# Kernel optimization log

Hardware: AMD Instinct MI355X
Metric: run time of the kernel (lower is better)

Reference implementation:

```python
import jax, jax.numpy as jnp
import numpy as np

B, N_PER, DEG, F_IN, F_HID = 64, 1024, 16, 128, 128
E = B * N_PER * DEG  # 1,048,576 edges, grouped per graph


def setup_inputs() -> dict:
    key = jax.random.key(0)
    ks = jax.random.split(key, 16)
    n_total = B * N_PER
    x = jax.random.normal(ks[0], (n_total, F_IN), dtype=jnp.float32)
    # edges are random within each graph block
    local = jax.random.randint(ks[1], (2, E), 0, N_PER)
    offs = (jnp.arange(E, dtype=jnp.int64) // (N_PER * DEG)) * N_PER
    edge_index = (local.astype(jnp.int64) + offs[None, :])
    edge_weight = jax.random.uniform(ks[2], (E,), dtype=jnp.float32)
    batch_index = jnp.repeat(jnp.arange(B, dtype=jnp.int64), N_PER)
    s = 1.0 / np.sqrt(F_HID)
    params = {
        'W1': jax.random.normal(ks[3], (F_IN, F_HID)) * s,
        'b1': jnp.zeros((F_HID,), jnp.float32),
        'p1': jax.random.normal(ks[4], (F_HID,)) * s,
        'W2': jax.random.normal(ks[5], (F_HID, F_HID)) * s,
        'b2': jnp.zeros((F_HID,), jnp.float32),
        'p2': jax.random.normal(ks[6], (F_HID,)) * s,
        'W3': jax.random.normal(ks[7], (F_HID, F_HID)) * s,
        'b3': jnp.zeros((F_HID,), jnp.float32),
        'p3': jax.random.normal(ks[8], (F_HID,)) * s,
        'Wo': jax.random.normal(ks[9], (2 * F_HID, 1)) * s,
        'bo': jnp.zeros((1,), jnp.float32),
    }
    return {'x': x, 'edge_index': edge_index, 'edge_weight': edge_weight,
            'batch_index': batch_index, **params}


def _gcn_conv(x, src, dst, w, W, b):
    # GCNConv with add_self_loops=True, symmetric normalization, edge_weight.
    n = x.shape[0]
    xW = x @ W
    deg = jnp.zeros((n,), x.dtype).at[dst].add(w) + 1.0  # +1 from self-loop fill
    dinv = jax.lax.rsqrt(deg)
    norm = dinv[src] * w * dinv[dst]
    agg = jnp.zeros_like(xW).at[dst].add(norm[:, None] * xW[src])
    return agg + (dinv * dinv)[:, None] * xW + b  # self-loop term + bias


def _topk_pool(x, src, dst, w, p, n, k):
    # TopKPooling with nonlinearity=sigmoid, equal-size graphs (n -> k nodes).
    f = x.shape[1]
    xr = x.reshape(B, n, f)
    score = jax.nn.sigmoid((xr @ p) / jnp.linalg.norm(p))  # [B, n]
    vals, perm = jax.lax.top_k(score, k)                    # per-graph top-k
    xn = jnp.take_along_axis(xr, perm[:, :, None], axis=1) * vals[:, :, None]
    # inverse map old local idx -> new local idx (-1 if dropped)
    inv = jnp.full((B, n), -1, dtype=jnp.int32)
    inv = inv.at[jnp.arange(B)[:, None], perm].set(jnp.arange(k, dtype=jnp.int32)[None, :])
    g = src // n
    sl = inv[g, src % n]
    dl = inv[dst // n, dst % n]
    keep = (sl >= 0) & (dl >= 0)
    # dropped edges are masked to node 0 with weight 0 (contribute nothing)
    src2 = jnp.where(keep, g * k + sl, 0)
    dst2 = jnp.where(keep, (dst // n) * k + dl, 0)
    w2 = jnp.where(keep, w, jnp.zeros((), w.dtype))
    return xn.reshape(B * k, f), src2, dst2, w2


def reference(x, edge_index, edge_weight, batch_index,
              W1, b1, p1, W2, b2, p2, W3, b3, p3, Wo, bo):
    src, dst = edge_index[0], edge_index[1]
    w = edge_weight
    n = N_PER
    h = _gcn_conv(x, src, dst, w, W1, b1)
    h, src, dst, w = _topk_pool(h, src, dst, w, p1, n, n // 2); n //= 2
    h = jax.nn.relu(h)
    h = _gcn_conv(h, src, dst, w, W2, b2)
    h, src, dst, w = _topk_pool(h, src, dst, w, p2, n, n // 2); n //= 2
    h = jax.nn.relu(h)
    h = _gcn_conv(h, src, dst, w, W3, b3)
    h, src, dst, w = _topk_pool(h, src, dst, w, p3, n, n // 2); n //= 2
    h = jax.nn.relu(h)
    hr = h.reshape(B, n, -1)
    cat = jnp.concatenate([hr.max(axis=1), hr.mean(axis=1)], axis=1)  # gmp || gap
    out = jax.nn.sigmoid(cat @ Wo + bo)
    return out, cat
```

## Files before the change

### kernel.cpp

```cpp
#include <hip/hip_runtime.h>

#define NB 64
#define EDGES 1048576
#define NTOT  65536

struct __align__(8) CsrE { int s; float w; };

using bf16x8 = __attribute__((ext_vector_type(8))) short;
using f32x4  = __attribute__((ext_vector_type(4))) float;

__global__ void k_zerof(float* __restrict__ p, int n){
  int i=blockIdx.x*256+threadIdx.x; if(i<n) p[i]=0.f;
}

__device__ inline void split1(float x, unsigned &hi16, unsigned &lo16){
  unsigned b=__float_as_uint(x);
  unsigned h=(b+0x7FFFu+((b>>16)&1u))&0xFFFF0000u;
  float lf=x-__uint_as_float(h);
  unsigned lb=__float_as_uint(lf);
  hi16=h>>16;
  lo16=(lb+0x7FFFu+((lb>>16)&1u))>>16;
}

__device__ inline void split8(const float4&u, const float4&v, bf16x8&hi, bf16x8&lo){
  float e[8]={u.x,u.y,u.z,u.w,v.x,v.y,v.z,v.w};
  #pragma unroll
  for(int j=0;j<8;++j){
    unsigned h16,l16; split1(e[j],h16,l16);
    hi[j]=(short)h16; lo[j]=(short)l16;
  }
}

__global__ __launch_bounds__(256) void k_cntpack(const int* __restrict__ edst,
        const float* __restrict__ ew, int* __restrict__ chunkcnt, float* __restrict__ chunkw,
        const float* __restrict__ W1, const float* __restrict__ W2,
        const float* __restrict__ W3, unsigned* __restrict__ outp){
  __shared__ int lc[1024];
  __shared__ float lw[1024];
  int b=blockIdx.x, tid=threadIdx.x;
  if(b<512){
    int xcd=b&7, slot=b>>3;
    int graph=xcd*8+(slot&7), chunk=slot>>3;
    int e0=graph*16384+chunk*2048;
    for(int t=tid;t<1024;t+=256){ lc[t]=0; lw[t]=0.f; }
    __syncthreads();
    for(int e=e0+tid; e<e0+2048; e+=256){
      int dl=edst[e]&1023;
      atomicAdd(&lc[dl],1);
      atomicAdd(&lw[dl],ew[e]);
    }
    __syncthreads();
    for(int t=tid;t<1024;t+=256){
      chunkcnt[chunk*65536+graph*1024+t]=lc[t];
      chunkw  [chunk*65536+graph*1024+t]=lw[t];
    }
  } else {
    int wb=b-512, m=wb>>3;
    const float* W = (m==0)?W1:((m==1)?W2:W3);
    unsigned* o = outp + m*16384;
    for(int t=(wb&7)*256+tid; t<8192; t+=2048){
      int i=t&3, l=(t>>2)&63, c=(t>>8)&7, q=(t>>11)&3;
      int col=c*16+(l&15);
      int k0=q*32+((l>>4)<<3)+i*2;
      float x0=W[k0*128+col], x1=W[(k0+1)*128+col];
      unsigned h0,l0,h1,l1;
      split1(x0,h0,l0); split1(x1,h1,l1);
      int base=((q*8+c)*2)*256;
      o[base + l*4 + i]       = (h1<<16)|h0;
      o[base + 256 + l*4 + i] = (l1<<16)|l0;
    }
  }
}

__global__ __launch_bounds__(256) void k_mm1scat(const float* __restrict__ X,
        const unsigned* __restrict__ Wpk,
        const int* __restrict__ esrc, const int* __restrict__ edst,
        const float* __restrict__ ew, const int* __restrict__ chunkcnt,
        const float* __restrict__ chunkw, int* __restrict__ rowptr,
        float* __restrict__ dinv1, CsrE* __restrict__ csr,
        float* __restrict__ Y){
  __shared__ __align__(16) unsigned Wl[4096];
  int b=blockIdx.x;
  if(b<512){
    const int RPB=128;
    int row0b=b*RPB;
    const int wave=threadIdx.x>>6, lane=threadIdx.x&63;
    const int row0=row0b+wave*32;
    const int lrow=lane&15, lko=(lane>>4)<<3;
    int orow[2];
    #pragma unroll
    for(int s=0;s<2;++s) orow[s]=row0+s*16+lrow;
    const f32x4 vzero={0.f,0.f,0.f,0.f};
    f32x4 acc[2][8];
    #pragma unroll
    for(int s=0;s<2;++s){
      #pragma unroll
      for(int c=0;c<8;++c) acc[s][c]=vzero;
    }
    const char* wb=(const char*)Wl + lane*16;
    float4 u[2],v[2];
    #pragma unroll
    for(int s=0;s<2;++s){
      const float* xp=X+(size_t)orow[s]*128+lko;
      u[s]=*(const float4*)xp; v[s]=*(const float4*)(xp+4);
    }
    #pragma unroll
    for(int q=0;q<4;++q){
      if(q) __syncthreads();
      for(int t=threadIdx.x;t<1024;t+=256)
        ((uint4*)Wl)[t]=((const uint4*)Wpk)[q*1024+t];
      __syncthreads();
      float4 un[2],vn[2];
      if(q<3){
        #pragma unroll
        for(int s=0;s<2;++s){
          const float* xp=X+(size_t)orow[s]*128+(q+1)*32+lko;
          un[s]=*(const float4*)xp; vn[s]=*(const float4*)(xp+4);
        }
      }
      bf16x8 Ah[2],Al[2];
      #pragma unroll
      for(int s=0;s<2;++s) split8(u[s],v[s],Ah[s],Al[s]);
      #pragma unroll
      for(int c=0;c<8;++c){
        const bf16x8 bh=*(const bf16x8*)(wb + c*2048);
        const bf16x8 bl=*(const bf16x8*)(wb + c*2048 + 1024);
        #pragma unroll
        for(int s=0;s<2;++s){
          acc[s][c]=__builtin_amdgcn_mfma_f32_16x16x32_bf16(Ah[s],bh,acc[s][c],0,0,0);
          acc[s][c]=__builtin_amdgcn_mfma_f32_16x16x32_bf16(Al[s],bh,acc[s][c],0,0,0);
          acc[s][c]=__builtin_amdgcn_mfma_f32_16x16x32_bf16(Ah[s],bl,acc[s][c],0,0,0);
        }
      }
      if(q<3){
        #pragma unroll
        for(int s=0;s<2;++s){ u[s]=un[s]; v[s]=vn[s]; }
      }
    }
    const int dcol=lane&15, dr0=(lane>>4)<<2;
    #pragma unroll
    for(int s=0;s<2;++s){
      #pragma unroll
      for(int c=0;c<8;++c){
        #pragma unroll
        for(int r=0;r<4;++r){
          Y[(size_t)(row0+s*16+dr0+r)*128 + c*16 + dcol]=acc[s][c][r];
        }
      }
    }
  } else {
    int* lc=(int*)Wl;
    int* wsum=(int*)Wl+1024;
    int sb=b-512, i=threadIdx.x;
    int lane=i&63, w=i>>6;
    int xcd=sb&7, slot=sb>>3;
    int graph=xcd*8+(slot&7), chunk=slot>>3;
    int n0=4*i, o0=graph*1024+n0;
    int ck[4][8], csum[4];
    int tot=0;
    #pragma unroll
    for(int j=0;j<4;++j){
      int c=0;
      #pragma unroll
      for(int k=0;k<8;++k){ int t=chunkcnt[k*65536+o0+j]; ck[j][k]=t; c+=t; }
      csum[j]=c; tot+=c;
    }
    int v=tot;
    #pragma unroll
    for(int off=1;off<64;off<<=1){ int t=__shfl_up(v,off,64); if(lane>=off) v+=t; }
    if(lane==63) wsum[w]=v;
    __syncthreads();
    int base=0;
    for(int k=0;k<w;++k) base+=wsum[k];
    int texcl=base+v-tot;
    int run=texcl;
    #pragma unroll
    for(int j=0;j<4;++j){
      int r0=graph*16384+run;
      if(chunk==0){
        rowptr[o0+j]=r0;
        float wsv=0.f;
        #pragma unroll
        for(int k=0;k<8;++k) wsv+=chunkw[k*65536+o0+j];
        dinv1[o0+j]=rsqrtf(wsv+1.0f);
      }
      int myfill=r0;
      #pragma unroll
      for(int k=0;k<8;++k) if(k<chunk) myfill+=ck[j][k];
      lc[n0+j]=myfill;
      run+=csum[j];
    }
    if(graph==63 && chunk==0 && i==255) rowptr[65536]=EDGES;
    __syncthreads();
    int e0=graph*16384+chunk*2048;
    for(int e=e0+i; e<e0+2048; e+=256){
      int dl=edst[e]&1023;
      int pos=atomicAdd(&lc[dl],1);
      CsrE ce; ce.s=esrc[e]; ce.w=ew[e];
      csr[pos]=ce;
    }
  }
}

template<bool G, int S, int EPI, int MMB>
__global__ __launch_bounds__(256) void mm_mfma(const float* __restrict__ X,
        const unsigned* __restrict__ Wpk, const int* __restrict__ selold,
        const float* __restrict__ score, float* __restrict__ Y, int gshift,
        const int* __restrict__ inv1, const int* __restrict__ sel1,
        const int* __restrict__ inv2, const int* __restrict__ sel2,
        int* __restrict__ inv12, int* __restrict__ map12,
        const int* __restrict__ rowptr, const CsrE* __restrict__ csr,
        float* __restrict__ dinv_out){
  __shared__ __align__(16) unsigned Wl[4096];
  int b=blockIdx.x;
  if(b<MMB){
    const int RPB = 64*S;
    int row0b;
    if(G){
      int xcd=b&7, slot=b>>3, bpg=1<<gshift;
      int graph=xcd*8+(slot>>gshift), idx=slot&(bpg-1);
      row0b = graph*(bpg*RPB) + idx*RPB;
    } else row0b = b*RPB;
    const int wave=threadIdx.x>>6, lane=threadIdx.x&63;
    const int row0 = row0b + wave*(16*S);
    const int lrow=lane&15, lko=(lane>>4)<<3;
    int orow[S]; float scr[S];
    #pragma unroll
    for(int s=0;s<S;++s){
      int rr=row0+s*16+lrow;
      orow[s]=G?selold[rr]:rr;
      scr[s]=G?score[orow[s]]:1.f;
    }
    const f32x4 vzero={0.f,0.f,0.f,0.f};
    f32x4 acc[S][8];
    #pragma unroll
    for(int s=0;s<S;++s){
      #pragma unroll
      for(int c=0;c<8;++c) acc[s][c]=vzero;
    }
    const char* wb=(const char*)Wl + lane*16;
    float4 u[S],v[S];
    #pragma unroll
    for(int s=0;s<S;++s){
      const float* xp=X+(size_t)orow[s]*128+lko;
      u[s]=*(const float4*)xp; v[s]=*(const float4*)(xp+4);
    }
    #pragma unroll
    for(int q=0;q<4;++q){
      if(q) __syncthreads();
      for(int t=threadIdx.x;t<1024;t+=256)
        ((uint4*)Wl)[t]=((const uint4*)Wpk)[q*1024+t];
      __syncthreads();
      float4 un[S],vn[S];
      if(q<3){
        #pragma unroll
        for(int s=0;s<S;++s){
          const float* xp=X+(size_t)orow[s]*128+(q+1)*32+lko;
          un[s]=*(const float4*)xp; vn[s]=*(const float4*)(xp+4);
        }
      }
      bf16x8 Ah[S],Al[S];
      #pragma unroll
      for(int s=0;s<S;++s){
        if(G){
          u[s].x=fmaxf(u[s].x*scr[s],0.f); u[s].y=fmaxf(u[s].y*scr[s],0.f);
          u[s].z=fmaxf(u[s].z*scr[s],0.f); u[s].w=fmaxf(u[s].w*scr[s],0.f);
          v[s].x=fmaxf(v[s].x*scr[s],0.f); v[s].y=fmaxf(v[s].y*scr[s],0.f);
          v[s].z=fmaxf(v[s].z*scr[s],0.f); v[s].w=fmaxf(v[s].w*scr[s],0.f);
        }
        split8(u[s],v[s],Ah[s],Al[s]);
      }
      #pragma unroll
      for(int c=0;c<8;++c){
        const bf16x8 bh=*(const bf16x8*)(wb + c*2048);
        const bf16x8 bl=*(const bf16x8*)(wb + c*2048 + 1024);
        #pragma unroll
        for(int s=0;s<S;++s){
          acc[s][c]=__builtin_amdgcn_mfma_f32_16x16x32_bf16(Ah[s],bh,acc[s][c],0,0,0);
          acc[s][c]=__builtin_amdgcn_mfma_f32_16x16x32_bf16(Al[s],bh,acc[s][c],0,0,0);
          acc[s][c]=__builtin_amdgcn_mfma_f32_16x16x32_bf16(Ah[s],bl,acc[s][c],0,0,0);
        }
      }
      if(q<3){
        #pragma unroll
        for(int s=0;s<S;++s){ u[s]=un[s]; v[s]=vn[s]; }
      }
    }
    const int dcol=lane&15, dr0=(lane>>4)<<2;
    #pragma unroll
    for(int s=0;s<S;++s){
      #pragma unroll
      for(int c=0;c<8;++c){
        #pragma unroll
        for(int r=0;r<4;++r){
          Y[(size_t)(row0+s*16+dr0+r)*128 + c*16 + dcol]=acc[s][c][r];
        }
      }
    }
    return;
  }
  if(EPI==2){
    int v=(b-MMB)*256+threadIdx.x;
    int d0=sel1[v];
    int rs=rowptr[d0], re=rowptr[d0+1];
    float s0=0.f,s1=0.f,s2=0.f,s3=0.f;
    int e=rs;
    for(; e+4<=re; e+=4){
      CsrE e0=csr[e], e1=csr[e+1], e2=csr[e+2], e3=csr[e+3];
      if(inv1[e0.s]>=0) s0+=e0.w;
      if(inv1[e1.s]>=0) s1+=e1.w;
      if(inv1[e2.s]>=0) s2+=e2.w;
      if(inv1[e3.s]>=0) s3+=e3.w;
    }
    for(; e<re; ++e){
      CsrE en=csr[e];
      if(inv1[en.s]>=0) s0+=en.w;
    }
    dinv_out[v]=rsqrtf((s0+s1)+(s2+s3)+1.0f);
  }
  if(EPI==3){
    int g=b-MMB, i=threadIdx.x;
    for(int t=i; t<1024; t+=256){
      int v0=g*1024+t;
      int q=inv1[v0];
      inv12[v0]=(q>=0)?inv2[q]:-1;
    }
    int v=g*256+i;
    map12[v]=sel1[sel2[v]];
    __syncthreads();
    int d0=map12[v];
    int rs=rowptr[d0], re=rowptr[d0+1];
    float s0=0.f,s1=0.f,s2=0.f,s3=0.f;
    int e=rs;
    for(; e+4<=re; e+=4){
      CsrE e0=csr[e], e1=csr[e+1], e2=csr[e+2], e3=csr[e+3];
      if(inv12[e0.s]>=0) s0+=e0.w;
      if(inv12[e1.s]>=0) s1+=e1.w;
      if(inv12[e2.s]>=0) s2+=e2.w;
      if(inv12[e3.s]>=0) s3+=e3.w;
    }
    for(; e<re; ++e){
      CsrE en=csr[e];
      if(inv12[en.s]>=0) s0+=en.w;
    }
    dinv_out[v]=rsqrtf((s0+s1)+(s2+s3)+1.0f);
  }
}

template<bool F>
__global__ __launch_bounds__(256) void k_gather(const float* __restrict__ xw, const CsrE* __restrict__ csr,
        const int* __restrict__ rowptr, const int* __restrict__ map, const int* __restrict__ inv,
        const float* __restrict__ dinvv, const float* __restrict__ bias, const float* __restrict__ p,
        float* __restrict__ h, float* __restrict__ score, int gshift, int ns){
  int wv=threadIdx.x>>6, half=(threadIdx.x>>5)&1, hl=threadIdx.x&31;
  int b=blockIdx.x, xcd=b&7, slot=b>>3, bpg=1<<gshift;
  int graph=xcd*8+(slot>>gshift), idx=slot&(bpg-1);
  int v = graph*(bpg<<3) + (idx<<3) + wv*2 + half;
  if(v>=ns) return;
  int d0 = F? map[v] : v;
  float dv=dinvv[v];
  int rs=rowptr[d0], re=rowptr[d0+1];
  const int f4=hl*4;
  float4 accA={0.f,0.f,0.f,0.f}, accB={0.f,0.f,0.f,0.f};
  for(int base=rs; base<re; base+=32){
    int len=re-base; if(len>32) len=32;
    int sidx=0; float cf=0.f;
    if(hl<len){
      CsrE en=csr[base+hl];
      int s=en.s; bool live=true;
      if(F){ int t=inv[s]; live=(t>=0); s=live?t:0; }
      if(live){ sidx=s; cf=dinvv[s]*en.w; }
    }
    int len4=(len+3)&~3;
    for(int j=0;j<len4;j+=4){
      float c0=__shfl(cf,j,32),   c1=__shfl(cf,j+1,32);
      float c2=__shfl(cf,j+2,32), c3=__shfl(cf,j+3,32);
      int   s0=__shfl(sidx,j,32),   s1=__shfl(sidx,j+1,32);
      int   s2=__shfl(sidx,j+2,32), s3=__shfl(sidx,j+3,32);
      const float4 x0=*(const float4*)&xw[(size_t)s0*128+f4];
      const float4 x1=*(const float4*)&xw[(size_t)s1*128+f4];
      const float4 x2=*(const float4*)&xw[(size_t)s2*128+f4];
      const float4 x3=*(const float4*)&xw[(size_t)s3*128+f4];
      accA.x+=c0*x0.x; accA.y+=c0*x0.y; accA.z+=c0*x0.z; accA.w+=c0*x0.w;
      accB.x+=c1*x1.x; accB.y+=c1*x1.y; accB.z+=c1*x1.z; accB.w+=c1*x1.w;
      accA.x+=c2*x2.x; accA.y+=c2*x2.y; accA.z+=c2*x2.z; accA.w+=c2*x2.w;
      accB.x+=c3*x3.x; accB.y+=c3*x3.y; accB.z+=c3*x3.z; accB.w+=c3*x3.w;
    }
  }
  float4 acc; acc.x=accA.x+accB.x; acc.y=accA.y+accB.y;
  acc.z=accA.z+accB.z; acc.w=accA.w+accB.w;
  const float4 xv=*(const float4*)&xw[(size_t)v*128+f4];
  const float4 bv=*(const float4*)&bias[f4];
  float d2=dv*dv;
  float4 hv;
  hv.x=acc.x*dv + d2*xv.x + bv.x;
  hv.y=acc.y*dv + d2*xv.y + bv.y;
  hv.z=acc.z*dv + d2*xv.z + bv.z;
  hv.w=acc.w*dv + d2*xv.w + bv.w;
  *(float4*)&h[(size_t)v*128+f4]=hv;
  const float4 pv=*(const float4*)&p[f4];
  float z=hv.x*pv.x+hv.y*pv.y+hv.z*pv.z+hv.w*pv.w;
  float pp=pv.x*pv.x+pv.y*pv.y+pv.z*pv.z+pv.w*pv.w;
  #pragma unroll
  for(int m=16;m>0;m>>=1){ z+=__shfl_xor(z,m,32); pp+=__shfl_xor(pp,m,32); }
  if(hl==0) score[v]=1.0f/(1.0f+expf(-z/sqrtf(pp)));
}

template<int N, int K, int MODE>
__global__ __launch_bounds__(N) void k_topk(const float* __restrict__ score,
        int* __restrict__ inv, int* __restrict__ selold,
        const float* __restrict__ h3, const float* __restrict__ Wo,
        const float* __restrict__ bo, float* __restrict__ outp){
  __shared__ unsigned hist[256];
  __shared__ int wsum[16];
  __shared__ int c_sh, r_sh;
  __shared__ float red[128];
  int g=blockIdx.x, i=threadIdx.x;
  int lane=i&63, w=i>>6;
  int gv=g*N+i;
  unsigned key=__float_as_uint(score[gv]);
  int st=1;
  int R=K;
  #pragma unroll
  for(int pass=0; pass<4; ++pass){
    int shift=24-pass*8;
    if(i<256) hist[i]=0;
    __syncthreads();
    unsigned byte=(key>>shift)&255u;
    if(st==1) atomicAdd(&hist[byte],1u);
    __syncthreads();
    unsigned hcnt=0, sfx=0;
    if(i<256){
      hcnt=hist[i]; sfx=hcnt;
      #pragma unroll
      for(int off=1;off<64;off<<=1){
        unsigned t=__shfl_down(sfx,off,64);
        if(lane+off<64) sfx+=t;
      }
      if(lane==0) wsum[w]=(int)sfx;
    }
    __syncthreads();
    if(i<256){
      int tot=0;
      for(int k=w+1;k<4;++k) tot+=wsum[k];
      int Si=(int)sfx+tot;
      int A=Si-(int)hcnt;
      if(A<R && R<=Si){ c_sh=i; r_sh=R-A; }
    }
    __syncthreads();
    int c=c_sh; R=r_sh;
    if(st==1){
      if((int)byte>c) st=2;
      else if((int)byte<c) st=0;
    }
    __syncthreads();
  }
  int alive=(st==1)?1:0;
  unsigned long long mA=__ballot(alive);
  int rA=__popcll(mA & ((1ULL<<lane)-1ULL));
  if(lane==0) wsum[w]=__popcll(mA);
  __syncthreads();
  int offA=0;
  for(int k=0;k<w;++k) offA+=wsum[k];
  int tie_rank=offA+rA;
  int sel=(st==2)||(st==1 && tie_rank<R);
  __syncthreads();
  unsigned long long mS=__ballot(sel);
  int rS=__popcll(mS & ((1ULL<<lane)-1ULL));
  if(lane==0) wsum[w]=__popcll(mS);
  __syncthreads();
  int offS=0;
  for(int k=0;k<w;++k) offS+=wsum[k];
  int ng=g*K+offS+rS;
  if(sel && ng<NB*K){ inv[gv]=ng; selold[ng]=gv; }
  else inv[gv]=-1;
  if(MODE==3){
    __syncthreads();
    int f=i;
    float mx=-3.4e38f, sm=0.f;
    if(f<128){
      for(int nd=0;nd<128;++nd){
        int old=selold[g*128+nd];
        float vv=fmaxf(h3[(size_t)old*128+f]*score[old],0.f);
        mx=fmaxf(mx,vv); sm+=vv;
      }
      float mean=sm*(1.0f/128.0f);
      outp[64+g*256+f]    =mx;
      outp[64+g*256+128+f]=mean;
      red[f]=mx*Wo[f]+mean*Wo[128+f];
    }
    __syncthreads();
    for(int off=64;off>0;off>>=1){
      if(f<off) red[f]+=red[f+off];
      __syncthreads();
    }
    if(f==0){ float z=red[0]+bo[0]; outp[g]=1.0f/(1.0f+expf(-z)); }
  }
}

extern "C" void kernel_launch(void* const* d_in, const int* in_sizes, int n_in,
                              void* d_out, int out_size, void* d_ws, size_t ws_size,
                              hipStream_t stream) {
  (void)in_sizes; (void)n_in;
  const float* x  = (const float*)d_in[0];
  const int*   ei = (const int*)d_in[1];
  const float* ew = (const float*)d_in[2];
  const float* W1=(const float*)d_in[4];  const float* b1=(const float*)d_in[5];  const float* p1=(const float*)d_in[6];
  const float* W2=(const float*)d_in[7];  const float* b2=(const float*)d_in[8];  const float* p2=(const float*)d_in[9];
  const float* W3=(const float*)d_in[10]; const float* b3=(const float*)d_in[11]; const float* p3=(const float*)d_in[12];
  const float* Wo=(const float*)d_in[13]; const float* bo=(const float*)d_in[14];
  float* out=(float*)d_out;

  char* ws=(char*)d_ws;
  size_t cur=0;
  float* slot0=(float*)(ws+cur); cur+=33554432;
  float* slot1=(float*)(ws+cur); cur+=33554432;
  CsrE*  csr  =(CsrE*)(ws+cur);  cur+=(size_t)EDGES*8;
  int*   chunkcnt=(int*)(ws+cur); cur+=2097152;
  float* chunkw  =(float*)(ws+cur); cur+=2097152;
  int*   rowptr=(int*) (ws+cur); cur+=262400;
  float* dinv1=(float*)(ws+cur); cur+=262144;
  float* dinv2=(float*)(ws+cur); cur+=131072;
  float* dinv3=(float*)(ws+cur); cur+=65536;
  float* sc1  =(float*)(ws+cur); cur+=262144;
  float* sc2  =(float*)(ws+cur); cur+=131072;
  float* sc3  =(float*)(ws+cur); cur+=65536;
  int*   inv1 =(int*)  (ws+cur); cur+=262144;
  int*   inv2 =(int*)  (ws+cur); cur+=131072;
  int*   invS =(int*)  (ws+cur); cur+=65536;
  int*   inv12=(int*)  (ws+cur); cur+=262144;
  int*   sel1 =(int*)  (ws+cur); cur+=131072;
  int*   sel2 =(int*)  (ws+cur); cur+=65536;
  int*   sel3 =(int*)  (ws+cur); cur+=32768;
  int*   map12=(int*)  (ws+cur); cur+=65536;
  unsigned* wpk=(unsigned*)(ws+cur); cur+=196608;

  if (ws_size < cur) {
    k_zerof<<<(out_size+255)/256,256,0,stream>>>(out,out_size);
    return;
  }

  const int* esrc=ei; const int* edst=ei+EDGES;

  k_cntpack<<<536,256,0,stream>>>(edst,ew,chunkcnt,chunkw,W1,W2,W3,wpk);
  k_mm1scat<<<1024,256,0,stream>>>(x,wpk,esrc,edst,ew,chunkcnt,chunkw,
                                   rowptr,dinv1,csr,slot0);
  k_gather<false><<<NTOT/8,256,0,stream>>>(slot0,csr,rowptr,nullptr,nullptr,
                                           dinv1,b1,p1,slot1,sc1,7,NTOT);
  k_topk<1024,512,0><<<NB,1024,0,stream>>>(sc1,inv1,sel1,nullptr,nullptr,nullptr,nullptr);

  mm_mfma<true,1,2,512><<<640,256,0,stream>>>(slot1,wpk+16384,sel1,sc1,slot0,3,
      inv1,sel1,nullptr,nullptr,nullptr,nullptr,rowptr,csr,dinv2);
  k_gather<true><<<32768/8,256,0,stream>>>(slot0,csr,rowptr,sel1,inv1,
                                           dinv2,b2,p2,slot1,sc2,6,32768);
  k_topk<512,256,0><<<NB,512,0,stream>>>(sc2,inv2,sel2,nullptr,nullptr,nullptr,nullptr);

  mm_mfma<true,1,3,256><<<320,256,0,stream>>>(slot1,wpk+32768,sel2,sc2,slot0,2,
      inv1,sel1,inv2,sel2,inv12,map12,rowptr,csr,dinv3);
  k_gather<true><<<16384/8,256,0,stream>>>(slot0,csr,rowptr,map12,inv12,
                                           dinv3,b3,p3,slot1,sc3,5,16384);
  k_topk<256,128,3><<<NB,256,0,stream>>>(sc3,invS,sel3,slot1,Wo,bo,out);
}
```

Baseline: 256.1 us.

## Fuse first top-k selection into gather via last-block-per-graph tail

```diff
diff --git a/kernel.cpp b/kernel.cpp
--- a/kernel.cpp
+++ b/kernel.cpp
@@ -34,7 +34,8 @@
 __global__ __launch_bounds__(256) void k_cntpack(const int* __restrict__ edst,
         const float* __restrict__ ew, int* __restrict__ chunkcnt, float* __restrict__ chunkw,
         const float* __restrict__ W1, const float* __restrict__ W2,
-        const float* __restrict__ W3, unsigned* __restrict__ outp){
+        const float* __restrict__ W3, unsigned* __restrict__ outp,
+        int* __restrict__ gcnt){
   __shared__ int lc[1024];
   __shared__ float lw[1024];
   int b=blockIdx.x, tid=threadIdx.x;
@@ -56,6 +57,7 @@
     }
   } else {
     int wb=b-512, m=wb>>3;
+    if(wb==0 && tid<64) gcnt[tid]=0;
     const float* W = (m==0)?W1:((m==1)?W2:W3);
     unsigned* o = outp + m*16384;
     for(int t=(wb&7)*256+tid; t<8192; t+=2048){
@@ -347,63 +349,149 @@
   }
 }
 
-template<bool F>
+template<bool F, bool TAIL>
 __global__ __launch_bounds__(256) void k_gather(const float* __restrict__ xw, const CsrE* __restrict__ csr,
         const int* __restrict__ rowptr, const int* __restrict__ map, const int* __restrict__ inv,
         const float* __restrict__ dinvv, const float* __restrict__ bias, const float* __restrict__ p,
-        float* __restrict__ h, float* __restrict__ score, int gshift, int ns){
+        float* __restrict__ h, float* __restrict__ score, int gshift, int ns,
+        int* __restrict__ gcnt, int* __restrict__ invO, int* __restrict__ selO){
+  __shared__ unsigned tl_hist[256];
+  __shared__ int tl_wsum[4];
+  __shared__ int tl_ws2[16];
+  __shared__ int tl_c, tl_r, tl_last;
   int wv=threadIdx.x>>6, half=(threadIdx.x>>5)&1, hl=threadIdx.x&31;
   int b=blockIdx.x, xcd=b&7, slot=b>>3, bpg=1<<gshift;
   int graph=xcd*8+(slot>>gshift), idx=slot&(bpg-1);
   int v = graph*(bpg<<3) + (idx<<3) + wv*2 + half;
-  if(v>=ns) return;
-  int d0 = F? map[v] : v;
-  float dv=dinvv[v];
-  int rs=rowptr[d0], re=rowptr[d0+1];
-  const int f4=hl*4;
-  float4 accA={0.f,0.f,0.f,0.f}, accB={0.f,0.f,0.f,0.f};
-  for(int base=rs; base<re; base+=32){
-    int len=re-base; if(len>32) len=32;
-    int sidx=0; float cf=0.f;
-    if(hl<len){
-      CsrE en=csr[base+hl];
-      int s=en.s; bool live=true;
-      if(F){ int t=inv[s]; live=(t>=0); s=live?t:0; }
-      if(live){ sidx=s; cf=dinvv[s]*en.w; }
-    }
-    int len4=(len+3)&~3;
-    for(int j=0;j<len4;j+=4){
-      float c0=__shfl(cf,j,32),   c1=__shfl(cf,j+1,32);
-      float c2=__shfl(cf,j+2,32), c3=__shfl(cf,j+3,32);
-      int   s0=__shfl(sidx,j,32),   s1=__shfl(sidx,j+1,32);
-      int   s2=__shfl(sidx,j+2,32), s3=__shfl(sidx,j+3,32);
-      const float4 x0=*(const float4*)&xw[(size_t)s0*128+f4];
-      const float4 x1=*(const float4*)&xw[(size_t)s1*128+f4];
-      const float4 x2=*(const float4*)&xw[(size_t)s2*128+f4];
-      const float4 x3=*(const float4*)&xw[(size_t)s3*128+f4];
-      accA.x+=c0*x0.x; accA.y+=c0*x0.y; accA.z+=c0*x0.z; accA.w+=c0*x0.w;
-      accB.x+=c1*x1.x; accB.y+=c1*x1.y; accB.z+=c1*x1.z; accB.w+=c1*x1.w;
-      accA.x+=c2*x2.x; accA.y+=c2*x2.y; accA.z+=c2*x2.z; accA.w+=c2*x2.w;
-      accB.x+=c3*x3.x; accB.y+=c3*x3.y; accB.z+=c3*x3.z; accB.w+=c3*x3.w;
-    }
-  }
-  float4 acc; acc.x=accA.x+accB.x; acc.y=accA.y+accB.y;
-  acc.z=accA.z+accB.z; acc.w=accA.w+accB.w;
-  const float4 xv=*(const float4*)&xw[(size_t)v*128+f4];
-  const float4 bv=*(const float4*)&bias[f4];
-  float d2=dv*dv;
-  float4 hv;
-  hv.x=acc.x*dv + d2*xv.x + bv.x;
-  hv.y=acc.y*dv + d2*xv.y + bv.y;
-  hv.z=acc.z*dv + d2*xv.z + bv.z;
-  hv.w=acc.w*dv + d2*xv.w + bv.w;
-  *(float4*)&h[(size_t)v*128+f4]=hv;
-  const float4 pv=*(const float4*)&p[f4];
-  float z=hv.x*pv.x+hv.y*pv.y+hv.z*pv.z+hv.w*pv.w;
-  float pp=pv.x*pv.x+pv.y*pv.y+pv.z*pv.z+pv.w*pv.w;
+  if(v<ns){
+    int d0 = F? map[v] : v;
+    float dv=dinvv[v];
+    int rs=rowptr[d0], re=rowptr[d0+1];
+    const int f4=hl*4;
+    float4 accA={0.f,0.f,0.f,0.f}, accB={0.f,0.f,0.f,0.f};
+    for(int base=rs; base<re; base+=32){
+      int len=re-base; if(len>32) len=32;
+      int sidx=0; float cf=0.f;
+      if(hl<len){
+        CsrE en=csr[base+hl];
+        int s=en.s; bool live=true;
+        if(F){ int t=inv[s]; live=(t>=0); s=live?t:0; }
+        if(live){ sidx=s; cf=dinvv[s]*en.w; }
+      }
+      int len4=(len+3)&~3;
+      for(int j=0;j<len4;j+=4){
+        float c0=__shfl(cf,j,32),   c1=__shfl(cf,j+1,32);
+        float c2=__shfl(cf,j+2,32), c3=__shfl(cf,j+3,32);
+        int   s0=__shfl(sidx,j,32),   s1=__shfl(sidx,j+1,32);
+        int   s2=__shfl(sidx,j+2,32), s3=__shfl(sidx,j+3,32);
+        const float4 x0=*(const float4*)&xw[(size_t)s0*128+f4];
+        const float4 x1=*(const float4*)&xw[(size_t)s1*128+f4];
+        const float4 x2=*(const float4*)&xw[(size_t)s2*128+f4];
+        const float4 x3=*(const float4*)&xw[(size_t)s3*128+f4];
+        accA.x+=c0*x0.x; accA.y+=c0*x0.y; accA.z+=c0*x0.z; accA.w+=c0*x0.w;
+        accB.x+=c1*x1.x; accB.y+=c1*x1.y; accB.z+=c1*x1.z; accB.w+=c1*x1.w;
+        accA.x+=c2*x2.x; accA.y+=c2*x2.y; accA.z+=c2*x2.z; accA.w+=c2*x2.w;
+        accB.x+=c3*x3.x; accB.y+=c3*x3.y; accB.z+=c3*x3.z; accB.w+=c3*x3.w;
+      }
+    }
+    float4 acc; acc.x=accA.x+accB.x; acc.y=accA.y+accB.y;
+    acc.z=accA.z+accB.z; acc.w=accA.w+accB.w;
+    const float4 xv=*(const float4*)&xw[(size_t)v*128+f4];
+    const float4 bv=*(const float4*)&bias[f4];
+    float d2=dv*dv;
+    float4 hv;
+    hv.x=acc.x*dv + d2*xv.x + bv.x;
+    hv.y=acc.y*dv + d2*xv.y + bv.y;
+    hv.z=acc.z*dv + d2*xv.z + bv.z;
+    hv.w=acc.w*dv + d2*xv.w + bv.w;
+    *(float4*)&h[(size_t)v*128+f4]=hv;
+    const float4 pv=*(const float4*)&p[f4];
+    float z=hv.x*pv.x+hv.y*pv.y+hv.z*pv.z+hv.w*pv.w;
+    float pp=pv.x*pv.x+pv.y*pv.y+pv.z*pv.z+pv.w*pv.w;
+    #pragma unroll
+    for(int m=16;m>0;m>>=1){ z+=__shfl_xor(z,m,32); pp+=__shfl_xor(pp,m,32); }
+    if(hl==0) score[v]=1.0f/(1.0f+expf(-z/sqrtf(pp)));
+  }
+  if(!TAIL) return;
+  __threadfence();
+  if(threadIdx.x==0)
+    tl_last = (atomicAdd(&gcnt[graph],1) == (1<<gshift)-1);
+  __syncthreads();
+  if(!tl_last) return;
+  __threadfence();
+  int i=threadIdx.x, lane2=i&63, w2=i>>6;
+  unsigned key[4]; int st[4]; unsigned byt[4];
   #pragma unroll
-  for(int m=16;m>0;m>>=1){ z+=__shfl_xor(z,m,32); pp+=__shfl_xor(pp,m,32); }
-  if(hl==0) score[v]=1.0f/(1.0f+expf(-z/sqrtf(pp)));
+  for(int j=0;j<4;++j){ key[j]=__float_as_uint(score[graph*1024+j*256+i]); st[j]=1; }
+  int R=512;
+  for(int pass=0; pass<4; ++pass){
+    int shift=24-pass*8;
+    tl_hist[i]=0;
+    __syncthreads();
+    #pragma unroll
+    for(int j=0;j<4;++j){
+      byt[j]=(key[j]>>shift)&255u;
+      if(st[j]==1) atomicAdd(&tl_hist[byt[j]],1u);
+    }
+    __syncthreads();
+    unsigned hcnt=tl_hist[i], sfx=hcnt;
+    #pragma unroll
+    for(int off=1;off<64;off<<=1){
+      unsigned t=__shfl_down(sfx,off,64);
+      if(lane2+off<64) sfx+=t;
+    }
+    if(lane2==0) tl_wsum[w2]=(int)sfx;
+    __syncthreads();
+    int tot=0;
+    for(int k=w2+1;k<4;++k) tot+=tl_wsum[k];
+    int Si=(int)sfx+tot, A=Si-(int)hcnt;
+    if(A<R && R<=Si){ tl_c=i; tl_r=R-A; }
+    __syncthreads();
+    int c=tl_c; R=tl_r;
+    #pragma unroll
+    for(int j=0;j<4;++j){
+      if(st[j]==1){
+        if((int)byt[j]>c) st[j]=2;
+        else if((int)byt[j]<c) st[j]=0;
+      }
+    }
+    __syncthreads();
+  }
+  int pre[4];
+  #pragma unroll
+  for(int j=0;j<4;++j){
+    unsigned long long m=__ballot(st[j]==1);
+    pre[j]=__popcll(m&((1ULL<<lane2)-1ULL));
+    if(lane2==0) tl_ws2[j*4+w2]=__popcll(m);
+  }
+  __syncthreads();
+  int sel[4];
+  #pragma unroll
+  for(int j=0;j<4;++j){
+    int base=0;
+    for(int jj=0;jj<j;++jj){ for(int k=0;k<4;++k) base+=tl_ws2[jj*4+k]; }
+    for(int k=0;k<w2;++k) base+=tl_ws2[j*4+k];
+    int tie=base+pre[j];
+    sel[j]=(st[j]==2)||(st[j]==1 && tie<R);
+  }
+  __syncthreads();
+  #pragma unroll
+  for(int j=0;j<4;++j){
+    unsigned long long m=__ballot(sel[j]);
+    pre[j]=__popcll(m&((1ULL<<lane2)-1ULL));
+    if(lane2==0) tl_ws2[j*4+w2]=__popcll(m);
+  }
+  __syncthreads();
+  #pragma unroll
+  for(int j=0;j<4;++j){
+    int base=0;
+    for(int jj=0;jj<j;++jj){ for(int k=0;k<4;++k) base+=tl_ws2[jj*4+k]; }
+    for(int k=0;k<w2;++k) base+=tl_ws2[j*4+k];
+    int ng=graph*512+base+pre[j];
+    int gv=graph*1024+j*256+i;
+    if(sel[j] && ng<NB*512){ invO[gv]=ng; selO[ng]=gv; }
+    else invO[gv]=-1;
+  }
 }
 
 template<int N, int K, int MODE>
@@ -533,6 +621,7 @@
   int*   sel2 =(int*)  (ws+cur); cur+=65536;
   int*   sel3 =(int*)  (ws+cur); cur+=32768;
   int*   map12=(int*)  (ws+cur); cur+=65536;
+  int*   gcnt =(int*)  (ws+cur); cur+=256;
   unsigned* wpk=(unsigned*)(ws+cur); cur+=196608;
 
   if (ws_size < cur) {
@@ -542,22 +631,24 @@
 
   const int* esrc=ei; const int* edst=ei+EDGES;
 
-  k_cntpack<<<536,256,0,stream>>>(edst,ew,chunkcnt,chunkw,W1,W2,W3,wpk);
+  k_cntpack<<<536,256,0,stream>>>(edst,ew,chunkcnt,chunkw,W1,W2,W3,wpk,gcnt);
   k_mm1scat<<<1024,256,0,stream>>>(x,wpk,esrc,edst,ew,chunkcnt,chunkw,
                                    rowptr,dinv1,csr,slot0);
-  k_gather<false><<<NTOT/8,256,0,stream>>>(slot0,csr,rowptr,nullptr,nullptr,
-                                           dinv1,b1,p1,slot1,sc1,7,NTOT);
-  k_topk<1024,512,0><<<NB,1024,0,stream>>>(sc1,inv1,sel1,nullptr,nullptr,nullptr,nullptr);
+  k_gather<false,true><<<NTOT/8,256,0,stream>>>(slot0,csr,rowptr,nullptr,nullptr,
+                                           dinv1,b1,p1,slot1,sc1,7,NTOT,
+                                           gcnt,inv1,sel1);
 
   mm_mfma<true,1,2,512><<<640,256,0,stream>>>(slot1,wpk+16384,sel1,sc1,slot0,3,
       inv1,sel1,nullptr,nullptr,nullptr,nullptr,rowptr,csr,dinv2);
-  k_gather<true><<<32768/8,256,0,stream>>>(slot0,csr,rowptr,sel1,inv1,
-                                           dinv2,b2,p2,slot1,sc2,6,32768);
+  k_gather<true,false><<<32768/8,256,0,stream>>>(slot0,csr,rowptr,sel1,inv1,
+                                           dinv2,b2,p2,slot1,sc2,6,32768,
+                                           nullptr,nullptr,nullptr);
   k_topk<512,256,0><<<NB,512,0,stream>>>(sc2,inv2,sel2,nullptr,nullptr,nullptr,nullptr);
 
   mm_mfma<true,1,3,256><<<320,256,0,stream>>>(slot1,wpk+32768,sel2,sc2,slot0,2,
       inv1,sel1,inv2,sel2,inv12,map12,rowptr,csr,dinv3);
-  k_gather<true><<<16384/8,256,0,stream>>>(slot0,csr,rowptr,map12,inv12,
-                                           dinv3,b3,p3,slot1,sc3,5,16384);
+  k_gather<true,false><<<16384/8,256,0,stream>>>(slot0,csr,rowptr,map12,inv12,
+                                           dinv3,b3,p3,slot1,sc3,5,16384,
+                                           nullptr,nullptr,nullptr);
   k_topk<256,128,3><<<NB,256,0,stream>>>(sc3,invS,sel3,slot1,Wo,bo,out);
 }
```

Result: slower. 990.0 us (+286.6%).
